# Optimization experiments

Hardware: AMD Instinct MI355X
Metric: run time of the kernel (lower is better)

## Reference

```python
import jax, jax.numpy as jnp
import numpy as np

DIM = 768
N_HEADS = 12
HEAD_DIM = DIM // N_HEADS
MAX_REL = 3  # hardcoded in the module


def setup_inputs() -> dict:
    key = jax.random.key(0)
    ks = jax.random.split(key, 10)
    B, L = 4, 1024
    def xavier(k, shape):
        fan_in, fan_out = shape[-2], shape[-1]
        a = jnp.sqrt(6.0 / (fan_in + fan_out))
        return jax.random.uniform(k, shape, jnp.float32, -a, a)
    return {
        "query": jax.random.normal(ks[0], (B, L, DIM), jnp.float32),
        "key":   jax.random.normal(ks[1], (B, L, DIM), jnp.float32),
        "value": jax.random.normal(ks[2], (B, L, DIM), jnp.float32),
        "Wq": xavier(ks[3], (DIM, DIM)),
        "Wk": xavier(ks[4], (DIM, DIM)),
        "Wv": xavier(ks[5], (DIM, DIM)),
        "Wproj": xavier(ks[6], (DIM, DIM)),
        "b_proj": jnp.zeros((DIM,), jnp.float32),
        "rel_k_table": xavier(ks[7], (2 * MAX_REL + 1, HEAD_DIM)),
        "rel_v_table": xavier(ks[8], (2 * MAX_REL + 1, HEAD_DIM)),
    }


def _rel_embed(table, len_q, len_k):
    # [len_q, len_k, head_dim] gathered from clipped relative distances
    dist = jnp.arange(len_k)[None, :] - jnp.arange(len_q)[:, None]
    idx = jnp.clip(dist, -MAX_REL, MAX_REL) + MAX_REL
    return table[idx]


def reference(query, key, value, Wq, Wk, Wv, Wproj, b_proj, rel_k_table, rel_v_table):
    B, Lq, _ = query.shape
    Lk = key.shape[1]
    H, hd = N_HEADS, HEAD_DIM
    scale = hd ** (-0.5)

    q = query @ Wq.T                      # [B, Lq, D]
    k = key @ Wk.T                        # [B, Lk, D]
    v = value @ Wv.T                      # [B, Lk, D]

    qh = q.reshape(B, Lq, H, hd).transpose(0, 2, 1, 3)   # [B,H,Lq,hd]
    kh = k.reshape(B, Lk, H, hd).transpose(0, 2, 1, 3)
    vh = v.reshape(B, Lk, H, hd).transpose(0, 2, 1, 3)

    # content-content scores
    attn1 = jnp.einsum('bhqd,bhkd->bhqk', qh, kh)
    # content-relative-position scores
    rk = _rel_embed(rel_k_table, Lq, Lk)                  # [Lq,Lk,hd]
    attn2 = jnp.einsum('bhqd,qkd->bhqk', qh, rk)
    # NOTE: original code DIVIDES by scale (= hd**-0.5), i.e. multiplies by sqrt(hd)
    attn = (attn1 + attn2) / scale
    attn = jax.nn.softmax(attn, axis=-1)                  # [B,H,Lq,Lk]

    w1 = jnp.einsum('bhqk,bhkd->bhqd', attn, vh)
    rv = _rel_embed(rel_v_table, Lq, Lk)                  # [Lq,Lk,hd]
    w2 = jnp.einsum('bhqk,qkd->bhqd', attn, rv)

    x = (w1 + w2).transpose(0, 2, 1, 3).reshape(B, Lq, H * hd)
    x = x @ Wproj.T + b_proj
    return (x, attn)
```

## Files before the change

kernel.cpp:

```cpp
#include <hip/hip_runtime.h>

#define DIMM 768
#define NH 12
#define HD 64
#define LSEQ 1024
#define BATCH 4
#define NXE 3145728
#define NWE 589824

typedef __bf16 bf16x8 __attribute__((ext_vector_type(8)));
typedef float f32x4 __attribute__((ext_vector_type(4)));
typedef unsigned short u16;

static __device__ __forceinline__ u16 f2bf(float f) {
  unsigned u = __builtin_bit_cast(unsigned, f);
  u += 0x7fffu + ((u >> 16) & 1u);
  return (u16)(u >> 16);
}
static __device__ __forceinline__ float bf2f(u16 h) {
  unsigned u = ((unsigned)h) << 16;
  return __builtin_bit_cast(float, u);
}
static __device__ __forceinline__ bf16x8 ld8bf(const u16* p) {
  uint4 u = *(const uint4*)p;
  return __builtin_bit_cast(bf16x8, u);
}
#define MFMA(a, b, c) __builtin_amdgcn_mfma_f32_16x16x32_bf16(a, b, c, 0, 0, 0)
#define GLL(g, s)                                                      \
  __builtin_amdgcn_global_load_lds(                                    \
      (const __attribute__((address_space(1))) void*)(g),              \
      (__attribute__((address_space(3))) void*)(s), 16, 0, 0)

__global__ __launch_bounds__(256) void convert(
    const float* __restrict__ q_in, const float* __restrict__ k_in,
    const float* __restrict__ v_in, const float* __restrict__ Wq,
    const float* __restrict__ Wk, const float* __restrict__ Wv,
    const float* __restrict__ Wp, u16* __restrict__ AqH, u16* __restrict__ AqL,
    u16* __restrict__ AkH, u16* __restrict__ AkL, u16* __restrict__ Av,
    u16* __restrict__ WqH, u16* __restrict__ WqL, u16* __restrict__ WkH,
    u16* __restrict__ WkL, u16* __restrict__ Wvr, u16* __restrict__ Wpr) {
  long i = ((long)blockIdx.x * 256 + threadIdx.x) * 4;
  const float* src;
  u16 *dh, *dl = nullptr;
  long off;
  if (i < NXE) { src = q_in; dh = AqH; dl = AqL; off = i; }
  else if (i < 2L * NXE) { src = k_in; dh = AkH; dl = AkL; off = i - NXE; }
  else if (i < 3L * NXE) { src = v_in; dh = Av; off = i - 2L * NXE; }
  else {
    long j = i - 3L * NXE;
    int which = (int)(j / NWE);
    off = j % NWE;
    if (which == 0) { src = Wq; dh = WqH; dl = WqL; }
    else if (which == 1) { src = Wk; dh = WkH; dl = WkL; }
    else if (which == 2) { src = Wv; dh = Wvr; }
    else { src = Wp; dh = Wpr; }
  }
  float4 v = *(const float4*)(src + off);
  ushort4 h;
  h.x = f2bf(v.x); h.y = f2bf(v.y); h.z = f2bf(v.z); h.w = f2bf(v.w);
  *(ushort4*)(dh + off) = h;
  if (dl) {
    ushort4 lo;
    lo.x = f2bf(v.x - bf2f(h.x)); lo.y = f2bf(v.y - bf2f(h.y));
    lo.z = f2bf(v.z - bf2f(h.z)); lo.w = f2bf(v.w - bf2f(h.w));
    *(ushort4*)(dl + off) = lo;
  }
}

__global__ __launch_bounds__(256, 3) void gemm_multi(
    int mode0, const u16* __restrict__ AqH, const u16* __restrict__ AqL,
    const u16* __restrict__ AkH, const u16* __restrict__ AkL,
    const u16* __restrict__ Av, const u16* __restrict__ WqH,
    const u16* __restrict__ WqL, const u16* __restrict__ WkH,
    const u16* __restrict__ WkL, const u16* __restrict__ Wvr,
    const u16* __restrict__ Wpr, const u16* __restrict__ wbuf,
    u16* __restrict__ qhi, u16* __restrict__ qlo, u16* __restrict__ khi,
    u16* __restrict__ klo, u16* __restrict__ vT, float* __restrict__ outp,
    const float* __restrict__ bias) {
  __shared__ u16 sAh[128 * 32], sAl[128 * 32];
  __shared__ u16 sBh[128 * 32], sBl[128 * 32];
  const int mode = mode0 + blockIdx.z;
  const u16 *Ah, *Al = nullptr, *Bh, *Bl = nullptr;
  if (mode == 0) { Ah = AqH; Al = AqL; Bh = WqH; Bl = WqL; }
  else if (mode == 1) { Ah = AkH; Al = AkL; Bh = WkH; Bl = WkL; }
  else if (mode == 2) { Ah = Av; Bh = Wvr; }
  else { Ah = wbuf; Bh = Wpr; }
  const int t = threadIdx.x, w = t >> 6, l = t & 63;
  const int quad = l >> 4, l15 = l & 15;
  const int m0 = blockIdx.x * 128, n0 = blockIdx.y * 128;
  const int wm = (w >> 1) * 64, wn = (w & 1) * 64;
  const int srow = t >> 2, scol = (t & 3) * 8;
  const u16* gA = Ah + (m0 + srow) * DIMM + scol;
  const u16* gB = Bh + (n0 + srow) * DIMM + scol;
  u16* lA = sAh + w * 512;
  u16* lB = sBh + w * 512;
  f32x4 acc[4][4] = {};
  if (mode < 2) {
    const u16* gAl = Al + (m0 + srow) * DIMM + scol;
    const u16* gBl = Bl + (n0 + srow) * DIMM + scol;
    u16* lAl = sAl + w * 512;
    u16* lBl = sBl + w * 512;
    for (int k0 = 0; k0 < DIMM; k0 += 32) {
      GLL(gA + k0, lA);
      GLL(gA + 64 * DIMM + k0, lA + 2048);
      GLL(gAl + k0, lAl);
      GLL(gAl + 64 * DIMM + k0, lAl + 2048);
      GLL(gB + k0, lB);
      GLL(gB + 64 * DIMM + k0, lB + 2048);
      GLL(gBl + k0, lBl);
      GLL(gBl + 64 * DIMM + k0, lBl + 2048);
      __syncthreads();
      bf16x8 ah[4], bh[4], xl[4];
#pragma unroll
      for (int i = 0; i < 4; ++i)
        ah[i] = __builtin_bit_cast(
            bf16x8, *(const uint4*)(sAh + (wm + i * 16 + l15) * 32 + quad * 8));
#pragma unroll
      for (int j = 0; j < 4; ++j)
        bh[j] = __builtin_bit_cast(
            bf16x8, *(const uint4*)(sBh + (wn + j * 16 + l15) * 32 + quad * 8));
#pragma unroll
      for (int i = 0; i < 4; ++i)
#pragma unroll
        for (int j = 0; j < 4; ++j) acc[i][j] = MFMA(ah[i], bh[j], acc[i][j]);
#pragma unroll
      for (int i = 0; i < 4; ++i)
        xl[i] = __builtin_bit_cast(
            bf16x8, *(const uint4*)(sAl + (wm + i * 16 + l15) * 32 + quad * 8));
#pragma unroll
      for (int i = 0; i < 4; ++i)
#pragma unroll
        for (int j = 0; j < 4; ++j) acc[i][j] = MFMA(xl[i], bh[j], acc[i][j]);
#pragma unroll
      for (int j = 0; j < 4; ++j)
        xl[j] = __builtin_bit_cast(
            bf16x8, *(const uint4*)(sBl + (wn + j * 16 + l15) * 32 + quad * 8));
#pragma unroll
      for (int i = 0; i < 4; ++i)
#pragma unroll
        for (int j = 0; j < 4; ++j) acc[i][j] = MFMA(ah[i], xl[j], acc[i][j]);
      __syncthreads();
    }
  } else {
    for (int k0 = 0; k0 < DIMM; k0 += 32) {
      GLL(gA + k0, lA);
      GLL(gA + 64 * DIMM + k0, lA + 2048);
      GLL(gB + k0, lB);
      GLL(gB + 64 * DIMM + k0, lB + 2048);
      __syncthreads();
      bf16x8 ah[4], bh[4];
#pragma unroll
      for (int i = 0; i < 4; ++i)
        ah[i] = __builtin_bit_cast(
            bf16x8, *(const uint4*)(sAh + (wm + i * 16 + l15) * 32 + quad * 8));
#pragma unroll
      for (int j = 0; j < 4; ++j)
        bh[j] = __builtin_bit_cast(
            bf16x8, *(const uint4*)(sBh + (wn + j * 16 + l15) * 32 + quad * 8));
#pragma unroll
      for (int i = 0; i < 4; ++i)
#pragma unroll
        for (int j = 0; j < 4; ++j) acc[i][j] = MFMA(ah[i], bh[j], acc[i][j]);
      __syncthreads();
    }
  }
  u16* oh = (mode == 0) ? qhi : khi;
  u16* ol = (mode == 0) ? qlo : klo;
#pragma unroll
  for (int i = 0; i < 4; ++i)
#pragma unroll
    for (int j = 0; j < 4; ++j)
#pragma unroll
      for (int r = 0; r < 4; ++r) {
        int grow = m0 + wm + i * 16 + quad * 4 + r;
        int gcol = n0 + wn + j * 16 + l15;
        float c = acc[i][j][r];
        int b = grow >> 10, ll = grow & 1023, h = gcol >> 6, d = gcol & 63;
        if (mode < 2) {
          int idx = ((b * NH + h) * LSEQ + ll) * HD + d;
          u16 hi = f2bf(c);
          oh[idx] = hi;
          ol[idx] = f2bf(c - bf2f(hi));
        } else if (mode == 2) {
          vT[((b * NH + h) * HD + d) * LSEQ + ll] = f2bf(c);
        } else {
          outp[grow * DIMM + gcol] = c + bias[gcol];
        }
      }
}

__global__ __launch_bounds__(256, 3) void attn_core(
    const u16* __restrict__ qhi, const u16* __restrict__ qlo,
    const u16* __restrict__ khi, const u16* __restrict__ klo,
    const u16* __restrict__ vT, const float* __restrict__ relk,
    const float* __restrict__ relv, float* __restrict__ attn_out,
    u16* __restrict__ wbuf) {
  __shared__ __align__(16) u16 Pb[16][1032];
  __shared__ float qrel[16][7];
  __shared__ float arel[16][7];
  __shared__ float rvt[7][64];
  __shared__ float red[4][16][4];

  const int qt = blockIdx.x, h = blockIdx.y, b = blockIdx.z;
  const int q0 = qt * 16;
  const int tid = threadIdx.x, wave = tid >> 6, lane = tid & 63;
  const int quad = lane >> 4, l15 = lane & 15;
  const int bhd = b * NH + h;

  for (int t = tid; t < 7 * HD; t += 256) rvt[t >> 6][t & 63] = relv[t];
  if (tid < 112) {
    int q = tid / 7, rr = tid % 7;
    const u16* qp = qhi + (bhd * LSEQ + q0 + q) * HD;
    const u16* lp = qlo + (bhd * LSEQ + q0 + q) * HD;
    const float* tp = relk + rr * HD;
    float s = 0.f;
    for (int d = 0; d < HD; ++d) s += (bf2f(qp[d]) + bf2f(lp[d])) * tp[d];
    qrel[q][rr] = s;
    arel[q][rr] = 0.f;
  }
  __syncthreads();

  f32x4 sc[16];
  {
    const int qbase = (bhd * LSEQ + q0 + l15) * HD + quad * 8;
    bf16x8 ah0 = ld8bf(qhi + qbase);
    bf16x8 ah1 = ld8bf(qhi + qbase + 32);
    bf16x8 al0 = ld8bf(qlo + qbase);
    bf16x8 al1 = ld8bf(qlo + qbase + 32);
    const u16* bh = khi + (bhd * LSEQ + wave * 16 + l15) * HD + quad * 8;
    const u16* bl = klo + (bhd * LSEQ + wave * 16 + l15) * HD + quad * 8;
    bf16x8 kh0 = ld8bf(bh), kh1 = ld8bf(bh + 32);
    bf16x8 kl0 = ld8bf(bl), kl1 = ld8bf(bl + 32);
#pragma unroll
    for (int it = 0; it < 16; ++it) {
      bf16x8 nh0 = kh0, nh1 = kh1, nl0 = kl0, nl1 = kl1;
      if (it < 15) {
        const u16* ph = bh + (it + 1) * 4096;
        const u16* pl = bl + (it + 1) * 4096;
        nh0 = ld8bf(ph); nh1 = ld8bf(ph + 32);
        nl0 = ld8bf(pl); nl1 = ld8bf(pl + 32);
      }
      f32x4 acc = {};
      acc = MFMA(ah0, kh0, acc);
      acc = MFMA(ah1, kh1, acc);
      acc = MFMA(ah0, kl0, acc);
      acc = MFMA(ah1, kl1, acc);
      acc = MFMA(al0, kh0, acc);
      acc = MFMA(al1, kh1, acc);
      sc[it] = acc;
      kh0 = nh0; kh1 = nh1; kl0 = nl0; kl1 = nl1;
    }
  }

  const int colbase = wave * 16 + l15;
  const int dbase = colbase - q0 - quad * 4;
  float mrow[4] = {-3.4e38f, -3.4e38f, -3.4e38f, -3.4e38f};
#pragma unroll
  for (int it = 0; it < 16; ++it)
#pragma unroll
    for (int r = 0; r < 4; ++r) {
      int d = dbase + it * 64 - r;
      int ri = d < -3 ? 0 : (d > 3 ? 6 : d + 3);
      float s = (sc[it][r] + qrel[quad * 4 + r][ri]) * 8.0f;
      sc[it][r] = s;
      mrow[r] = fmaxf(mrow[r], s);
    }
#pragma unroll
  for (int m = 1; m <= 8; m <<= 1)
#pragma unroll
    for (int r = 0; r < 4; ++r) mrow[r] = fmaxf(mrow[r], __shfl_xor(mrow[r], m));
  if (l15 < 4) {
    float mv = l15 == 0 ? mrow[0] : l15 == 1 ? mrow[1] : l15 == 2 ? mrow[2] : mrow[3];
    red[0][quad * 4 + l15][wave] = mv;
  }
  __syncthreads();
  float mx[4];
#pragma unroll
  for (int r = 0; r < 4; ++r) {
    int row = quad * 4 + r;
    mx[r] = fmaxf(fmaxf(red[0][row][0], red[0][row][1]),
                  fmaxf(red[0][row][2], red[0][row][3]));
  }

  float sum[4] = {}, s0a[4] = {}, s6a[4] = {};
#pragma unroll
  for (int it = 0; it < 16; ++it)
#pragma unroll
    for (int r = 0; r < 4; ++r) {
      float e = __expf(sc[it][r] - mx[r]);
      sc[it][r] = e;
      int d = dbase + it * 64 - r;
      sum[r] += e;
      if (d <= -3) s0a[r] += e;
      if (d >= 3) s6a[r] += e;
    }
#pragma unroll
  for (int m = 1; m <= 8; m <<= 1)
#pragma unroll
    for (int r = 0; r < 4; ++r) {
      sum[r] += __shfl_xor(sum[r], m);
      s0a[r] += __shfl_xor(s0a[r], m);
      s6a[r] += __shfl_xor(s6a[r], m);
    }
  if (l15 < 4) {
    int row = quad * 4 + l15;
    float sv = l15 == 0 ? sum[0] : l15 == 1 ? sum[1] : l15 == 2 ? sum[2] : sum[3];
    float a0 = l15 == 0 ? s0a[0] : l15 == 1 ? s0a[1] : l15 == 2 ? s0a[2] : s0a[3];
    float a6 = l15 == 0 ? s6a[0] : l15 == 1 ? s6a[1] : l15 == 2 ? s6a[2] : s6a[3];
    red[1][row][wave] = sv;
    red[2][row][wave] = a0;
    red[3][row][wave] = a6;
  }
  __syncthreads();
  float rn[4];
#pragma unroll
  for (int r = 0; r < 4; ++r) {
    int row = quad * 4 + r;
    float s = red[1][row][0] + red[1][row][1] + red[1][row][2] + red[1][row][3];
    rn[r] = 1.0f / s;
    if (wave == 0 && l15 == 0) {
      float t0 = red[2][row][0] + red[2][row][1] + red[2][row][2] + red[2][row][3];
      float t6 = red[3][row][0] + red[3][row][1] + red[3][row][2] + red[3][row][3];
      arel[row][0] = t0 * rn[r];
      arel[row][6] = t6 * rn[r];
    }
  }

  float* aob = attn_out + ((size_t)(bhd * LSEQ + q0)) * LSEQ;
#pragma unroll
  for (int it = 0; it < 16; ++it) {
    int col = colbase + it * 64;
#pragma unroll
    for (int r = 0; r < 4; ++r) {
      int row = quad * 4 + r;
      float p = sc[it][r] * rn[r];
      aob[row * LSEQ + col] = p;
      Pb[row][col] = f2bf(p);
      int d = dbase + it * 64 - r;
      if (d >= -2 && d <= 2) arel[row][d + 3] = p;
    }
  }
  __syncthreads();

  {
    const u16* vb = vT + (bhd * HD + wave * 16 + l15) * LSEQ;
    f32x4 acc = {};
    for (int kk = 0; kk < LSEQ; kk += 32) {
      int ak = kk + quad * 8;
      bf16x8 aP = __builtin_bit_cast(bf16x8, *(const uint4*)&Pb[l15][ak]);
      bf16x8 bV = ld8bf(vb + ak);
      acc = MFMA(aP, bV, acc);
    }
    const int col = wave * 16 + l15;
#pragma unroll
    for (int r = 0; r < 4; ++r) {
      int row = quad * 4 + r;
      float w2 = 0.f;
#pragma unroll
      for (int t = 0; t < 7; ++t) w2 += arel[row][t] * rvt[t][col];
      wbuf[(b * LSEQ + q0 + row) * DIMM + h * HD + col] = f2bf(acc[r] + w2);
    }
  }
}

extern "C" void kernel_launch(void* const* d_in, const int* in_sizes, int n_in,
                              void* d_out, int out_size, void* d_ws, size_t ws_size,
                              hipStream_t stream) {
  const float* q_in = (const float*)d_in[0];
  const float* k_in = (const float*)d_in[1];
  const float* v_in = (const float*)d_in[2];
  const float* Wq = (const float*)d_in[3];
  const float* Wk = (const float*)d_in[4];
  const float* Wv = (const float*)d_in[5];
  const float* Wp = (const float*)d_in[6];
  const float* bias = (const float*)d_in[7];
  const float* relk = (const float*)d_in[8];
  const float* relv = (const float*)d_in[9];
  float* out = (float*)d_out;

  u16* p = (u16*)d_ws;
  u16 *AqH = p, *AqL = AqH + NXE, *AkH = AqL + NXE, *AkL = AkH + NXE,
      *Av = AkL + NXE;
  u16 *WqH = Av + NXE, *WqL = WqH + NWE, *WkH = WqL + NWE, *WkL = WkH + NWE,
      *Wvr = WkL + NWE, *Wpr = Wvr + NWE;
  u16 *qhi = Wpr + NWE, *qlo = qhi + NXE, *khi = qlo + NXE, *klo = khi + NXE,
      *vT = klo + NXE, *wbuf = vT + NXE;

  convert<<<(3 * NXE + 4 * NWE) / 1024, 256, 0, stream>>>(
      q_in, k_in, v_in, Wq, Wk, Wv, Wp, AqH, AqL, AkH, AkL, Av, WqH, WqL, WkH,
      WkL, Wvr, Wpr);
  gemm_multi<<<dim3(32, 6, 3), 256, 0, stream>>>(
      0, AqH, AqL, AkH, AkL, Av, WqH, WqL, WkH, WkL, Wvr, Wpr, wbuf, qhi, qlo,
      khi, klo, vT, out, bias);
  attn_core<<<dim3(64, NH, BATCH), 256, 0, stream>>>(
      qhi, qlo, khi, klo, vT, relk, relv, out + NXE, wbuf);
  gemm_multi<<<dim3(32, 6, 1), 256, 0, stream>>>(
      3, AqH, AqL, AkH, AkL, Av, WqH, WqL, WkH, WkL, Wvr, Wpr, wbuf, qhi, qlo,
      khi, klo, vT, out, bias);
}
```

Before: 467.4 us.

## Stage K tiles in LDS, write attn from bf16 buffer, vectorize qrel loads

The QK^T loop now loads each 64-row K hi/lo chunk cooperatively into a swizzled shared buffer through GLL (global-to-LDS) copies, with two barriers per chunk, instead of every wave reading K straight from global memory. Scores are split across two accumulators. The attention output is written as coalesced float4 rows read back from the shared bf16 P buffer instead of scattered scalar stores. The qrel dot product uses vector loads, and the PV loop is unrolled. The attention matrix written out is now rounded to bf16, which loses precision in the returned attn. The barrier after the qrel setup was removed and the kernel relies on the later per-chunk barriers.

```diff
diff --git a/kernel.cpp b/kernel.cpp
--- a/kernel.cpp
+++ b/kernel.cpp
@@ -195,7 +195,7 @@
     const u16* __restrict__ vT, const float* __restrict__ relk,
     const float* __restrict__ relv, float* __restrict__ attn_out,
     u16* __restrict__ wbuf) {
-  __shared__ __align__(16) u16 Pb[16][1032];
+  __shared__ __align__(16) u16 uni[16 * 1032];
   __shared__ float qrel[16][7];
   __shared__ float arel[16][7];
   __shared__ float rvt[7][64];
@@ -214,11 +214,24 @@
     const u16* lp = qlo + (bhd * LSEQ + q0 + q) * HD;
     const float* tp = relk + rr * HD;
     float s = 0.f;
-    for (int d = 0; d < HD; ++d) s += (bf2f(qp[d]) + bf2f(lp[d])) * tp[d];
+#pragma unroll
+    for (int d8 = 0; d8 < HD; d8 += 8) {
+      uint4 uh = *(const uint4*)(qp + d8);
+      uint4 ul = *(const uint4*)(lp + d8);
+      float4 t0 = *(const float4*)(tp + d8);
+      float4 t1 = *(const float4*)(tp + d8 + 4);
+      unsigned hh[4] = {uh.x, uh.y, uh.z, uh.w};
+      unsigned lv[4] = {ul.x, ul.y, ul.z, ul.w};
+      float tv[8] = {t0.x, t0.y, t0.z, t0.w, t1.x, t1.y, t1.z, t1.w};
+#pragma unroll
+      for (int m = 0; m < 4; ++m) {
+        s += (bf2f((u16)(hh[m] & 0xffff)) + bf2f((u16)(lv[m] & 0xffff))) * tv[2 * m];
+        s += (bf2f((u16)(hh[m] >> 16)) + bf2f((u16)(lv[m] >> 16))) * tv[2 * m + 1];
+      }
+    }
     qrel[q][rr] = s;
     arel[q][rr] = 0.f;
   }
-  __syncthreads();
 
   f32x4 sc[16];
   {
@@ -227,28 +240,36 @@
     bf16x8 ah1 = ld8bf(qhi + qbase + 32);
     bf16x8 al0 = ld8bf(qlo + qbase);
     bf16x8 al1 = ld8bf(qlo + qbase + 32);
-    const u16* bh = khi + (bhd * LSEQ + wave * 16 + l15) * HD + quad * 8;
-    const u16* bl = klo + (bhd * LSEQ + wave * 16 + l15) * HD + quad * 8;
-    bf16x8 kh0 = ld8bf(bh), kh1 = ld8bf(bh + 32);
-    bf16x8 kl0 = ld8bf(bl), kl1 = ld8bf(bl + 32);
-#pragma unroll
-    for (int it = 0; it < 16; ++it) {
-      bf16x8 nh0 = kh0, nh1 = kh1, nl0 = kl0, nl1 = kl1;
-      if (it < 15) {
-        const u16* ph = bh + (it + 1) * 4096;
-        const u16* pl = bl + (it + 1) * 4096;
-        nh0 = ld8bf(ph); nh1 = ld8bf(ph + 32);
-        nl0 = ld8bf(pl); nl1 = ld8bf(pl + 32);
-      }
-      f32x4 acc = {};
-      acc = MFMA(ah0, kh0, acc);
-      acc = MFMA(ah1, kh1, acc);
-      acc = MFMA(ah0, kl0, acc);
-      acc = MFMA(ah1, kl1, acc);
-      acc = MFMA(al0, kh0, acc);
-      acc = MFMA(al1, kh1, acc);
-      sc[it] = acc;
-      kh0 = nh0; kh1 = nh1; kl0 = nl0; kl1 = nl1;
+    const int r = tid >> 3;
+    const int cg = (tid & 7) ^ (r & 7);
+    const u16* gh = khi + (bhd * LSEQ + r) * HD + cg * 8;
+    const u16* gl = klo + (bhd * LSEQ + r) * HD + cg * 8;
+    u16* sb = uni + wave * 512;
+    const int rowA = wave * 16 + l15;
+    const int sw = rowA & 7;
+    const int s0 = (rowA * 8 + (quad ^ sw)) * 8;
+    const int s1 = (rowA * 8 + ((quad + 4) ^ sw)) * 8;
+    for (int c = 0; c < 16; ++c) {
+      const u16* ghc = gh + c * 64 * HD;
+      const u16* glc = gl + c * 64 * HD;
+      GLL(ghc, sb);
+      GLL(ghc + 32 * HD, sb + 2048);
+      GLL(glc, sb + 4096);
+      GLL(glc + 32 * HD, sb + 6144);
+      __syncthreads();
+      bf16x8 kh0 = ld8bf(uni + s0);
+      bf16x8 kh1 = ld8bf(uni + s1);
+      bf16x8 kl0 = ld8bf(uni + 4096 + s0);
+      bf16x8 kl1 = ld8bf(uni + 4096 + s1);
+      f32x4 e = {}, f = {};
+      e = MFMA(ah0, kh0, e);
+      f = MFMA(ah1, kh1, f);
+      e = MFMA(ah0, kl0, e);
+      f = MFMA(ah1, kl1, f);
+      e = MFMA(al0, kh0, e);
+      f = MFMA(al1, kh1, f);
+      sc[c] = e + f;
+      __syncthreads();
     }
   }
 
@@ -256,13 +277,13 @@
   const int dbase = colbase - q0 - quad * 4;
   float mrow[4] = {-3.4e38f, -3.4e38f, -3.4e38f, -3.4e38f};
 #pragma unroll
-  for (int it = 0; it < 16; ++it)
+  for (int c = 0; c < 16; ++c)
 #pragma unroll
     for (int r = 0; r < 4; ++r) {
-      int d = dbase + it * 64 - r;
+      int d = dbase + c * 64 - r;
       int ri = d < -3 ? 0 : (d > 3 ? 6 : d + 3);
-      float s = (sc[it][r] + qrel[quad * 4 + r][ri]) * 8.0f;
-      sc[it][r] = s;
+      float s = (sc[c][r] + qrel[quad * 4 + r][ri]) * 8.0f;
+      sc[c][r] = s;
       mrow[r] = fmaxf(mrow[r], s);
     }
 #pragma unroll
@@ -284,12 +305,12 @@
 
   float sum[4] = {}, s0a[4] = {}, s6a[4] = {};
 #pragma unroll
-  for (int it = 0; it < 16; ++it)
+  for (int c = 0; c < 16; ++c)
 #pragma unroll
     for (int r = 0; r < 4; ++r) {
-      float e = __expf(sc[it][r] - mx[r]);
-      sc[it][r] = e;
-      int d = dbase + it * 64 - r;
+      float e = __expf(sc[c][r] - mx[r]);
+      sc[c][r] = e;
+      int d = dbase + c * 64 - r;
       sum[r] += e;
       if (d <= -3) s0a[r] += e;
       if (d >= 3) s6a[r] += e;
@@ -326,28 +347,38 @@
     }
   }
 
-  float* aob = attn_out + ((size_t)(bhd * LSEQ + q0)) * LSEQ;
-#pragma unroll
-  for (int it = 0; it < 16; ++it) {
-    int col = colbase + it * 64;
+#pragma unroll
+  for (int c = 0; c < 16; ++c) {
+    int col = colbase + c * 64;
 #pragma unroll
     for (int r = 0; r < 4; ++r) {
       int row = quad * 4 + r;
-      float p = sc[it][r] * rn[r];
-      aob[row * LSEQ + col] = p;
-      Pb[row][col] = f2bf(p);
-      int d = dbase + it * 64 - r;
+      float p = sc[c][r] * rn[r];
+      uni[row * 1032 + col] = f2bf(p);
+      int d = dbase + c * 64 - r;
       if (d >= -2 && d <= 2) arel[row][d + 3] = p;
     }
   }
   __syncthreads();
+
+  {
+    float* aob = attn_out + ((size_t)(bhd * LSEQ + q0)) * LSEQ;
+#pragma unroll
+    for (int row = 0; row < 16; ++row) {
+      uint2 u = *(const uint2*)&uni[row * 1032 + tid * 4];
+      float4 f = {bf2f((u16)(u.x & 0xffff)), bf2f((u16)(u.x >> 16)),
+                  bf2f((u16)(u.y & 0xffff)), bf2f((u16)(u.y >> 16))};
+      *(float4*)(aob + row * LSEQ + tid * 4) = f;
+    }
+  }
 
   {
     const u16* vb = vT + (bhd * HD + wave * 16 + l15) * LSEQ;
     f32x4 acc = {};
+#pragma unroll 4
     for (int kk = 0; kk < LSEQ; kk += 32) {
       int ak = kk + quad * 8;
-      bf16x8 aP = __builtin_bit_cast(bf16x8, *(const uint4*)&Pb[l15][ak]);
+      bf16x8 aP = __builtin_bit_cast(bf16x8, *(const uint4*)&uni[l15 * 1032 + ak]);
       bf16x8 bV = ld8bf(vb + ak);
       acc = MFMA(aP, bV, acc);
     }
```

Result: faster. 435.0 us (-6.9%).
